# Performance work log

Measured on AMD Instinct MI355X. Metric: run time of the kernel, lower is better.

Reference implementation:

```python
import jax, jax.numpy as jnp
import numpy as np

DIM, H, DH, MLP, ADIM = 512, 8, 64, 2048, 256
B, T = 4, 2048
EPS = 1e-5


def setup_inputs() -> dict:
    key = jax.random.key(0)
    ks = jax.random.split(key, 10)
    s = 0.02
    inner = H * DH
    return {
        "x": jax.random.normal(ks[0], (B, T, DIM), jnp.float32),
        "action_emb": jax.random.normal(ks[1], (B, T, ADIM), jnp.float32),
        "causal_mask": jnp.tril(jnp.ones((T, T), dtype=bool)),
        "Wqkv": jax.random.normal(ks[2], (3 * inner, DIM), jnp.float32) * s,
        "Wout": jax.random.normal(ks[3], (DIM, inner), jnp.float32) * s,
        "bout": jnp.zeros((DIM,), jnp.float32),
        "W1": jax.random.normal(ks[4], (MLP, DIM), jnp.float32) * s,
        "b1": jnp.zeros((MLP,), jnp.float32),
        "W2": jax.random.normal(ks[5], (DIM, MLP), jnp.float32) * s,
        "b2": jnp.zeros((DIM,), jnp.float32),
        # adaLN is zero-init in the module; use small random so modulation is exercised
        "Wmod": jax.random.normal(ks[6], (6 * DIM, ADIM), jnp.float32) * s,
        "bmod": jnp.zeros((6 * DIM,), jnp.float32),
    }


def _layernorm(z):
    mu = jnp.mean(z, axis=-1, keepdims=True)
    var = jnp.var(z, axis=-1, keepdims=True)
    return (z - mu) * jax.lax.rsqrt(var + EPS)


def reference(x, action_emb, causal_mask, Wqkv, Wout, bout, W1, b1, W2, b2, Wmod, bmod):
    b, t, d = x.shape
    mod = jax.nn.silu(action_emb) @ Wmod.T + bmod            # (B,T,6*dim)
    shift1, scale1, gate1, shift2, scale2, gate2 = jnp.split(mod, 6, axis=-1)

    h = _layernorm(x) * (1.0 + scale1) + shift1
    qkv = (h @ Wqkv.T).reshape(b, t, 3, H, DH)
    q, k, v = qkv[:, :, 0], qkv[:, :, 1], qkv[:, :, 2]        # (B,T,H,DH)
    scores = jnp.einsum("bqhd,bkhd->bhqk", q, k) * (DH ** -0.5)
    scores = jnp.where(causal_mask, scores, -jnp.inf)
    attn = jax.nn.softmax(scores, axis=-1)                   # dropout=eval (identity)
    h = jnp.einsum("bhqk,bkhd->bqhd", attn, v).reshape(b, t, H * DH)
    h = h @ Wout.T + bout
    x = x + gate1 * h

    h = _layernorm(x) * (1.0 + scale2) + shift2
    h = jax.nn.gelu(h @ W1.T + b1, approximate=False) @ W2.T + b2
    return x + gate2 * h
```

## Files before the change

### kernel.cpp

```cpp
#include <hip/hip_runtime.h>
#include <math.h>
#include <stdint.h>

#define BB 4
#define TT 2048
#define NTOK 8192
#define DIMD 512
#define HH 8
#define DHH 64
#define MLPD 2048
#define ADIMD 256
#define MODD 3072
#define LNEPS 1e-5f
#define LOG2E_8 0.18033688011112042f

typedef short short8 __attribute__((ext_vector_type(8)));
typedef unsigned short ushort4v __attribute__((ext_vector_type(4)));
typedef __bf16 bf16x8 __attribute__((ext_vector_type(8)));
typedef float f32x4 __attribute__((ext_vector_type(4)));

static __device__ __forceinline__ unsigned short f2bf(float f) {
    union { float f; unsigned u; } v; v.f = f;
    unsigned r = v.u + 0x7fffu + ((v.u >> 16) & 1u);
    return (unsigned short)(r >> 16);
}
static __device__ __forceinline__ float bf2f(unsigned short u) {
    union { unsigned u; float f; } v; v.u = (unsigned)u << 16; return v.f;
}

static __device__ __forceinline__ f32x4 mfma_bf16(short8 a, short8 b, f32x4 c) {
    return __builtin_amdgcn_mfma_f32_16x16x32_bf16(
        __builtin_bit_cast(bf16x8, a), __builtin_bit_cast(bf16x8, b), c, 0, 0, 0);
}

struct CvtArgs {
    const float* s[6];
    unsigned short* d[6];
    int cum[7];
};
__global__ __launch_bounds__(256) void cvt_all(CvtArgs a)
{
    const int i = blockIdx.x * 256 + threadIdx.x;
    if (i >= a.cum[6]) return;
    int seg = 0;
    #pragma unroll
    for (int k = 1; k < 6; k++) seg += (i >= a.cum[k]);
    const int off = i - a.cum[seg];
    float4 v = ((const float4*)a.s[seg])[off];
    if (seg == 5) {
        v.x = v.x / (1.f + __expf(-v.x));
        v.y = v.y / (1.f + __expf(-v.y));
        v.z = v.z / (1.f + __expf(-v.z));
        v.w = v.w / (1.f + __expf(-v.w));
    }
    ushort4v o = { f2bf(v.x), f2bf(v.y), f2bf(v.z), f2bf(v.w) };
    ((ushort4v*)a.d[seg])[off] = o;
}

template<int EPI, int BN>
__global__ __launch_bounds__(256) void gemm_bf16(
    const unsigned short* __restrict__ A, const unsigned short* __restrict__ Bw,
    const float* __restrict__ bias, const float* __restrict__ res,
    const unsigned short* __restrict__ mod,
    int M, int N, int K,
    void* __restrict__ Cv)
{
    constexpr int MT = (BN == 128) ? 4 : 2;
    constexpr int NPB = (BN == 128) ? 4 : 2;
    __shared__ unsigned short As[128 * 72];
    __shared__ unsigned short Bs[BN * 72];

    const int tid = threadIdx.x;
    const int w = tid >> 6, lane = tid & 63;
    const int quad = lane >> 4, l16 = lane & 15;
    const int wrow = (BN == 128) ? (w >> 1) * 64 : w * 32;
    const int wcol = (BN == 128) ? (w & 1) * 64 : 0;
    const int row0 = blockIdx.y * 128, col0 = blockIdx.x * BN;

    const int srow = tid >> 3;
    const int skc  = (tid & 7) * 8;

    f32x4 acc[MT][4];
    #pragma unroll
    for (int i = 0; i < MT; i++)
        #pragma unroll
        for (int j = 0; j < 4; j++) acc[i][j] = (f32x4){0.f, 0.f, 0.f, 0.f};

    short8 pA[4], pB[NPB];
    auto prefetch = [&](int k0) {
        #pragma unroll
        for (int p = 0; p < 4; p++)
            pA[p] = *(const short8*)&A[(size_t)(row0 + srow + p * 32) * K + k0 + skc];
        #pragma unroll
        for (int p = 0; p < NPB; p++)
            pB[p] = *(const short8*)&Bw[(size_t)(col0 + srow + p * 32) * K + k0 + skc];
    };
    auto stage = [&]() {
        #pragma unroll
        for (int p = 0; p < 4; p++)
            *(short8*)&As[(srow + p * 32) * 72 + skc] = pA[p];
        #pragma unroll
        for (int p = 0; p < NPB; p++)
            *(short8*)&Bs[(srow + p * 32) * 72 + skc] = pB[p];
    };

    prefetch(0);
    stage();
    __syncthreads();

    for (int k0 = 0; k0 < K; k0 += 64) {
        const bool more = (k0 + 64 < K);
        if (more) prefetch(k0 + 64);

        #pragma unroll
        for (int ks = 0; ks < 2; ks++) {
            short8 af[MT], bf[4];
            #pragma unroll
            for (int mt = 0; mt < MT; mt++)
                af[mt] = *(const short8*)&As[(wrow + mt * 16 + l16) * 72 + ks * 32 + quad * 8];
            #pragma unroll
            for (int nt = 0; nt < 4; nt++)
                bf[nt] = *(const short8*)&Bs[(wcol + nt * 16 + l16) * 72 + ks * 32 + quad * 8];
            #pragma unroll
            for (int nt = 0; nt < 4; nt++)
                #pragma unroll
                for (int mt = 0; mt < MT; mt++)
                    acc[mt][nt] = mfma_bf16(af[mt], bf[nt], acc[mt][nt]);
        }
        __syncthreads();
        if (more) stage();
        __syncthreads();
    }

    float* Cf = (float*)Cv;
    unsigned short* Cb = (unsigned short*)Cv;
    #pragma unroll
    for (int mt = 0; mt < MT; mt++) {
        #pragma unroll
        for (int r = 0; r < 4; r++) {
            const int row = row0 + wrow + mt * 16 + quad * 4 + r;
            #pragma unroll
            for (int nt = 0; nt < 4; nt++) {
                const int col = col0 + wcol + nt * 16 + l16;
                const size_t idx = (size_t)row * N + col;
                const float v = acc[mt][nt][r];
                if (EPI == 0) {
                    Cb[idx] = f2bf(v);
                } else if (EPI == 2) {
                    float t = v + bias[col];
                    Cb[idx] = f2bf(0.5f * t * (1.f + erff(t * 0.70710678118654752f)));
                } else if (EPI == 3) {
                    float t = v + bias[col];
                    Cf[idx] = res[idx] + bf2f(mod[(size_t)row * MODD + 1024 + col]) * t;
                } else if (EPI == 4) {
                    float t = v + bias[col];
                    Cf[idx] = Cf[idx] + bf2f(mod[(size_t)row * MODD + 2560 + col]) * t;
                } else if (EPI == 5) {
                    Cb[idx] = f2bf(v + bias[col]);
                }
            }
        }
    }
}

__global__ __launch_bounds__(256) void adaln_ln(
    const float* __restrict__ src, const unsigned short* __restrict__ mod,
    unsigned short* __restrict__ dst, int shift_off, int scale_off)
{
    const int n = blockIdx.x;
    const int tid = threadIdx.x;
    const float* xr = src + (size_t)n * DIMD;
    float v0 = xr[tid], v1 = xr[tid + 256];
    float s = v0 + v1;
    float q = v0 * v0 + v1 * v1;
    #pragma unroll
    for (int o = 32; o > 0; o >>= 1) {
        s += __shfl_down(s, o);
        q += __shfl_down(q, o);
    }
    __shared__ float sh[8];
    __shared__ float mu_sh, rs_sh;
    const int wid = tid >> 6, lane = tid & 63;
    if (lane == 0) { sh[wid] = s; sh[wid + 4] = q; }
    __syncthreads();
    if (tid == 0) {
        float S = sh[0] + sh[1] + sh[2] + sh[3];
        float Q = sh[4] + sh[5] + sh[6] + sh[7];
        float mu = S * (1.f / DIMD);
        float var = Q * (1.f / DIMD) - mu * mu;
        mu_sh = mu;
        rs_sh = rsqrtf(var + LNEPS);
    }
    __syncthreads();
    const float mu = mu_sh, rs = rs_sh;
    const unsigned short* mrow = mod + (size_t)n * MODD;
    const size_t o0 = (size_t)n * DIMD + tid;
    dst[o0]       = f2bf((v0 - mu) * rs * (1.f + bf2f(mrow[scale_off + tid]))       + bf2f(mrow[shift_off + tid]));
    dst[o0 + 256] = f2bf((v1 - mu) * rs * (1.f + bf2f(mrow[scale_off + tid + 256])) + bf2f(mrow[shift_off + tid + 256]));
}

__global__ __launch_bounds__(256, 2) void attn_mfma(
    const unsigned short* __restrict__ qkv, unsigned short* __restrict__ outb)
{
    __shared__ unsigned short Kt[128][72];
    __shared__ unsigned short Vt[64][136];
    __shared__ unsigned short Ps[4][32][136];

    const int qi = (TT / 128 - 1) - blockIdx.x;
    const int h = blockIdx.y, b = blockIdx.z;
    const int tid = threadIdx.x;
    const int w = tid >> 6;
    const int lane = tid & 63;
    const int quad = lane >> 4;
    const int l16 = lane & 15;

    const int qw = qi * 128 + w * 32;
    const size_t tokbase = (size_t)b * TT;

    short8 qf[2][2];
    #pragma unroll
    for (int nt = 0; nt < 2; nt++) {
        const unsigned short* qp = qkv + (tokbase + qw + nt * 16 + l16) * 1536 + h * 64 + quad * 8;
        #pragma unroll
        for (int hd = 0; hd < 2; hd++) {
            short8 raw = *(const short8*)(qp + hd * 32);
            short8 f;
            #pragma unroll
            for (int j = 0; j < 8; j++)
                f[j] = (short)f2bf(bf2f((unsigned short)raw[j]) * LOG2E_8);
            qf[nt][hd] = f;
        }
    }

    f32x4 Oa[4][2];
    float mrun[2] = {-INFINITY, -INFINITY}, lrun[2] = {0.f, 0.f};
    #pragma unroll
    for (int mt = 0; mt < 4; mt++)
        #pragma unroll
        for (int nt = 0; nt < 2; nt++) Oa[mt][nt] = (f32x4){0.f, 0.f, 0.f, 0.f};

    const int nkt = qi + 1;
    const int vk0 = (tid & 63) * 2;
    const int vdb = (tid >> 6) * 8;

    short8 kpre[4], vpre[4];
    auto prefetchKV = [&](int kt) {
        const unsigned short* kb = qkv + (tokbase + (size_t)kt * 128) * 1536 + 512 + h * 64;
        #pragma unroll
        for (int it = 0; it < 4; it++) {
            const int i = tid + it * 256;
            kpre[it] = *(const short8*)(kb + (size_t)(i >> 3) * 1536 + (i & 7) * 8);
        }
        const unsigned short* vb = qkv + (tokbase + (size_t)kt * 128 + vk0) * 1536 + 1024 + h * 64;
        #pragma unroll
        for (int p = 0; p < 2; p++) {
            vpre[2 * p]     = *(const short8*)(vb + p * 32 + vdb);
            vpre[2 * p + 1] = *(const short8*)(vb + 1536 + p * 32 + vdb);
        }
    };
    auto storeKV = [&]() {
        #pragma unroll
        for (int it = 0; it < 4; it++) {
            const int i = tid + it * 256;
            *(short8*)&Kt[i >> 3][(i & 7) * 8] = kpre[it];
        }
        #pragma unroll
        for (int p = 0; p < 2; p++)
            #pragma unroll
            for (int j = 0; j < 8; j++) {
                const int d = p * 32 + vdb + j;
                *(unsigned*)&Vt[d][vk0] =
                    (unsigned)(unsigned short)vpre[2 * p][j]
                    | ((unsigned)(unsigned short)vpre[2 * p + 1][j] << 16);
            }
    };

    prefetchKV(0);
    storeKV();
    __syncthreads();

    for (int kt = 0; kt < nkt; kt++) {
        const bool haveNext = (kt + 1 < nkt);
        if (haveNext) prefetchKV(kt + 1);

        short8 af[8][2];
        #pragma unroll
        for (int mk = 0; mk < 8; mk++) {
            af[mk][0] = *(const short8*)&Kt[mk * 16 + l16][quad * 8];
            af[mk][1] = *(const short8*)&Kt[mk * 16 + l16][32 + quad * 8];
        }
        #pragma unroll
        for (int nt = 0; nt < 2; nt++) {
            f32x4 st[8];
            #pragma unroll
            for (int mk = 0; mk < 8; mk++) {
                st[mk] = (f32x4){0.f, 0.f, 0.f, 0.f};
                st[mk] = mfma_bf16(af[mk][0], qf[nt][0], st[mk]);
                st[mk] = mfma_bf16(af[mk][1], qf[nt][1], st[mk]);
            }
            if (kt == qi) {
                const int qrel = w * 32 + nt * 16 + l16;
                #pragma unroll
                for (int mk = 0; mk < 8; mk++)
                    #pragma unroll
                    for (int r = 0; r < 4; r++)
                        if (mk * 16 + quad * 4 + r > qrel) st[mk][r] = -INFINITY;
            }
            float tm = -INFINITY;
            #pragma unroll
            for (int mk = 0; mk < 8; mk++)
                #pragma unroll
                for (int r = 0; r < 4; r++) tm = fmaxf(tm, st[mk][r]);
            tm = fmaxf(tm, __shfl_xor(tm, 16));
            tm = fmaxf(tm, __shfl_xor(tm, 32));
            const float mn = fmaxf(mrun[nt], tm);
            const float alpha = __builtin_amdgcn_exp2f(mrun[nt] - mn);
            mrun[nt] = mn;
            float ts = 0.f;
            #pragma unroll
            for (int mk = 0; mk < 8; mk++) {
                const float p0 = __builtin_amdgcn_exp2f(st[mk][0] - mn);
                const float p1 = __builtin_amdgcn_exp2f(st[mk][1] - mn);
                const float p2 = __builtin_amdgcn_exp2f(st[mk][2] - mn);
                const float p3 = __builtin_amdgcn_exp2f(st[mk][3] - mn);
                ts += (p0 + p1) + (p2 + p3);
                const unsigned long long pk =
                    (unsigned long long)f2bf(p0)
                    | ((unsigned long long)f2bf(p1) << 16)
                    | ((unsigned long long)f2bf(p2) << 32)
                    | ((unsigned long long)f2bf(p3) << 48);
                *(unsigned long long*)&Ps[w][nt * 16 + l16][mk * 16 + quad * 4] = pk;
            }
            ts += __shfl_xor(ts, 16);
            ts += __shfl_xor(ts, 32);
            lrun[nt] = lrun[nt] * alpha + ts;
            #pragma unroll
            for (int mt = 0; mt < 4; mt++) Oa[mt][nt] *= alpha;
        }
        __threadfence_block();

        short8 pf0[4], pf1[4];
        #pragma unroll
        for (int kc = 0; kc < 4; kc++) {
            pf0[kc] = *(const short8*)&Ps[w][l16][kc * 32 + quad * 8];
            pf1[kc] = *(const short8*)&Ps[w][16 + l16][kc * 32 + quad * 8];
        }
        #pragma unroll
        for (int mt = 0; mt < 4; mt++)
            #pragma unroll
            for (int kc = 0; kc < 4; kc++) {
                const short8 vf = *(const short8*)&Vt[mt * 16 + l16][kc * 32 + quad * 8];
                Oa[mt][0] = mfma_bf16(vf, pf0[kc], Oa[mt][0]);
                Oa[mt][1] = mfma_bf16(vf, pf1[kc], Oa[mt][1]);
            }

        __syncthreads();
        if (haveNext) storeKV();
        __syncthreads();
    }

    #pragma unroll
    for (int nt = 0; nt < 2; nt++) {
        const float inv = 1.f / lrun[nt];
        const size_t tok = tokbase + qw + nt * 16 + l16;
        #pragma unroll
        for (int mt = 0; mt < 4; mt++) {
            const unsigned long long pk =
                (unsigned long long)f2bf(Oa[mt][nt][0] * inv)
                | ((unsigned long long)f2bf(Oa[mt][nt][1] * inv) << 16)
                | ((unsigned long long)f2bf(Oa[mt][nt][2] * inv) << 32)
                | ((unsigned long long)f2bf(Oa[mt][nt][3] * inv) << 48);
            *(unsigned long long*)&outb[tok * DIMD + h * 64 + mt * 16 + quad * 4] = pk;
        }
    }
}

extern "C" void kernel_launch(void* const* d_in, const int* in_sizes, int n_in,
                              void* d_out, int out_size, void* d_ws, size_t ws_size,
                              hipStream_t stream)
{
    (void)in_sizes; (void)n_in; (void)out_size; (void)ws_size;

    const float* x    = (const float*)d_in[0];
    const float* aemb = (const float*)d_in[1];
    const float* Wqkv = (const float*)d_in[3];
    const float* Wout = (const float*)d_in[4];
    const float* bout = (const float*)d_in[5];
    const float* W1   = (const float*)d_in[6];
    const float* b1   = (const float*)d_in[7];
    const float* W2   = (const float*)d_in[8];
    const float* b2   = (const float*)d_in[9];
    const float* Wmod = (const float*)d_in[10];
    const float* bmod = (const float*)d_in[11];

    float* out = (float*)d_out;

    char* p = (char*)d_ws;
    unsigned short* modw = (unsigned short*)p; p += (size_t)NTOK * MODD * 2;
    unsigned short* h12  = (unsigned short*)p; p += (size_t)NTOK * DIMD * 2;
    unsigned short* qkvb = (unsigned short*)p; p += (size_t)NTOK * 1536 * 2;
    unsigned short* attw = (unsigned short*)p; p += (size_t)NTOK * DIMD * 2;
    unsigned short* hid  = qkvb;
    unsigned short* sact = (unsigned short*)p; p += (size_t)NTOK * ADIMD * 2;
    unsigned short* wq = (unsigned short*)p;   p += (size_t)1536 * 512 * 2;
    unsigned short* wo = (unsigned short*)p;   p += (size_t)512 * 512 * 2;
    unsigned short* w1 = (unsigned short*)p;   p += (size_t)2048 * 512 * 2;
    unsigned short* w2 = (unsigned short*)p;   p += (size_t)512 * 2048 * 2;
    unsigned short* wm = (unsigned short*)p;   p += (size_t)3072 * 256 * 2;

    CvtArgs ca;
    ca.s[0] = Wqkv; ca.d[0] = wq;
    ca.s[1] = Wout; ca.d[1] = wo;
    ca.s[2] = W1;   ca.d[2] = w1;
    ca.s[3] = W2;   ca.d[3] = w2;
    ca.s[4] = Wmod; ca.d[4] = wm;
    ca.s[5] = aemb; ca.d[5] = sact;
    const int n4s[6] = {1536 * 512 / 4, 512 * 512 / 4, 2048 * 512 / 4,
                        512 * 2048 / 4, 3072 * 256 / 4, NTOK * ADIMD / 4};
    ca.cum[0] = 0;
    for (int i = 0; i < 6; i++) ca.cum[i + 1] = ca.cum[i] + n4s[i];
    cvt_all<<<(ca.cum[6] + 255) / 256, 256, 0, stream>>>(ca);

    gemm_bf16<5, 128><<<dim3(MODD / 128, NTOK / 128), 256, 0, stream>>>(
        sact, wm, bmod, nullptr, nullptr, NTOK, MODD, ADIMD, modw);

    adaln_ln<<<NTOK, 256, 0, stream>>>(x, modw, h12, 0, 512);

    gemm_bf16<0, 128><<<dim3(1536 / 128, NTOK / 128), 256, 0, stream>>>(
        h12, wq, nullptr, nullptr, nullptr, NTOK, 1536, DIMD, qkvb);

    attn_mfma<<<dim3(TT / 128, HH, BB), 256, 0, stream>>>(qkvb, attw);

    gemm_bf16<3, 64><<<dim3(DIMD / 64, NTOK / 128), 256, 0, stream>>>(
        attw, wo, bout, x, modw, NTOK, DIMD, DIMD, out);

    adaln_ln<<<NTOK, 256, 0, stream>>>(out, modw, h12, 1536, 2048);

    gemm_bf16<2, 128><<<dim3(MLPD / 128, NTOK / 128), 256, 0, stream>>>(
        h12, w1, b1, nullptr, nullptr, NTOK, MLPD, DIMD, hid);

    gemm_bf16<4, 64><<<dim3(DIMD / 64, NTOK / 128), 256, 0, stream>>>(
        hid, w2, b2, nullptr, modw, NTOK, DIMD, MLPD, out);
}
```

Measured before the change: 338.1 us.

## Shrink attention tiles to 64 queries and 64 keys per block

Retiles the flash-attention kernel so each block handles 64 queries (16 per wave) and streams 64-key K/V tiles, instead of 128 queries with 128-key tiles. Shared memory and register use drop, launch bounds rise to 4 blocks per SM, and the grid doubles. The aim is more parallelism and occupancy with finer causal-diagonal waste. The trade-off is that each K/V tile is reused by half as many queries, so global K/V traffic and barrier count per FLOP go up.

```diff
diff --git a/kernel.cpp b/kernel.cpp
--- a/kernel.cpp
+++ b/kernel.cpp
@@ -199,14 +199,14 @@
     dst[o0 + 256] = f2bf((v1 - mu) * rs * (1.f + bf2f(mrow[scale_off + tid + 256])) + bf2f(mrow[shift_off + tid + 256]));
 }
 
-__global__ __launch_bounds__(256, 2) void attn_mfma(
+__global__ __launch_bounds__(256, 4) void attn_mfma(
     const unsigned short* __restrict__ qkv, unsigned short* __restrict__ outb)
 {
-    __shared__ unsigned short Kt[128][72];
-    __shared__ unsigned short Vt[64][136];
-    __shared__ unsigned short Ps[4][32][136];
-
-    const int qi = (TT / 128 - 1) - blockIdx.x;
+    __shared__ unsigned short Kt[64][72];
+    __shared__ unsigned short Vt[64][72];
+    __shared__ unsigned short Ps[4][16][72];
+
+    const int qi = (TT / 64 - 1) - blockIdx.x;
     const int h = blockIdx.y, b = blockIdx.z;
     const int tid = threadIdx.x;
     const int w = tid >> 6;
@@ -214,13 +214,12 @@
     const int quad = lane >> 4;
     const int l16 = lane & 15;
 
-    const int qw = qi * 128 + w * 32;
+    const int qw = qi * 64 + w * 16;
     const size_t tokbase = (size_t)b * TT;
 
-    short8 qf[2][2];
-    #pragma unroll
-    for (int nt = 0; nt < 2; nt++) {
-        const unsigned short* qp = qkv + (tokbase + qw + nt * 16 + l16) * 1536 + h * 64 + quad * 8;
+    short8 qf[2];
+    {
+        const unsigned short* qp = qkv + (tokbase + qw + l16) * 1536 + h * 64 + quad * 8;
         #pragma unroll
         for (int hd = 0; hd < 2; hd++) {
             short8 raw = *(const short8*)(qp + hd * 32);
@@ -228,51 +227,43 @@
             #pragma unroll
             for (int j = 0; j < 8; j++)
                 f[j] = (short)f2bf(bf2f((unsigned short)raw[j]) * LOG2E_8);
-            qf[nt][hd] = f;
-        }
-    }
-
-    f32x4 Oa[4][2];
-    float mrun[2] = {-INFINITY, -INFINITY}, lrun[2] = {0.f, 0.f};
+            qf[hd] = f;
+        }
+    }
+
+    f32x4 Oa[4];
+    float mrun = -INFINITY, lrun = 0.f;
     #pragma unroll
-    for (int mt = 0; mt < 4; mt++)
-        #pragma unroll
-        for (int nt = 0; nt < 2; nt++) Oa[mt][nt] = (f32x4){0.f, 0.f, 0.f, 0.f};
+    for (int mt = 0; mt < 4; mt++) Oa[mt] = (f32x4){0.f, 0.f, 0.f, 0.f};
 
     const int nkt = qi + 1;
-    const int vk0 = (tid & 63) * 2;
-    const int vdb = (tid >> 6) * 8;
-
-    short8 kpre[4], vpre[4];
+    const int vk0 = (tid & 31) * 2;
+    const int vdb = (tid >> 5) * 8;
+
+    short8 kpre[2], vpre[2];
     auto prefetchKV = [&](int kt) {
-        const unsigned short* kb = qkv + (tokbase + (size_t)kt * 128) * 1536 + 512 + h * 64;
-        #pragma unroll
-        for (int it = 0; it < 4; it++) {
+        const unsigned short* kb = qkv + (tokbase + (size_t)kt * 64) * 1536 + 512 + h * 64;
+        #pragma unroll
+        for (int it = 0; it < 2; it++) {
             const int i = tid + it * 256;
             kpre[it] = *(const short8*)(kb + (size_t)(i >> 3) * 1536 + (i & 7) * 8);
         }
-        const unsigned short* vb = qkv + (tokbase + (size_t)kt * 128 + vk0) * 1536 + 1024 + h * 64;
-        #pragma unroll
-        for (int p = 0; p < 2; p++) {
-            vpre[2 * p]     = *(const short8*)(vb + p * 32 + vdb);
-            vpre[2 * p + 1] = *(const short8*)(vb + 1536 + p * 32 + vdb);
-        }
+        const unsigned short* vb = qkv + (tokbase + (size_t)kt * 64 + vk0) * 1536 + 1024 + h * 64 + vdb;
+        vpre[0] = *(const short8*)vb;
+        vpre[1] = *(const short8*)(vb + 1536);
     };
     auto storeKV = [&]() {
         #pragma unroll
-        for (int it = 0; it < 4; it++) {
+        for (int it = 0; it < 2; it++) {
             const int i = tid + it * 256;
             *(short8*)&Kt[i >> 3][(i & 7) * 8] = kpre[it];
         }
         #pragma unroll
-        for (int p = 0; p < 2; p++)
-            #pragma unroll
-            for (int j = 0; j < 8; j++) {
-                const int d = p * 32 + vdb + j;
-                *(unsigned*)&Vt[d][vk0] =
-                    (unsigned)(unsigned short)vpre[2 * p][j]
-                    | ((unsigned)(unsigned short)vpre[2 * p + 1][j] << 16);
-            }
+        for (int j = 0; j < 8; j++) {
+            *(unsigned*)&Vt[vdb + j][vk0] =
+                (unsigned)(unsigned short)vpre[0][j]
+                | ((unsigned)(unsigned short)vpre[1][j] << 16);
+        }
     };
 
     prefetchKV(0);
@@ -283,75 +274,65 @@
         const bool haveNext = (kt + 1 < nkt);
         if (haveNext) prefetchKV(kt + 1);
 
-        short8 af[8][2];
-        #pragma unroll
-        for (int mk = 0; mk < 8; mk++) {
-            af[mk][0] = *(const short8*)&Kt[mk * 16 + l16][quad * 8];
-            af[mk][1] = *(const short8*)&Kt[mk * 16 + l16][32 + quad * 8];
-        }
-        #pragma unroll
-        for (int nt = 0; nt < 2; nt++) {
-            f32x4 st[8];
-            #pragma unroll
-            for (int mk = 0; mk < 8; mk++) {
-                st[mk] = (f32x4){0.f, 0.f, 0.f, 0.f};
-                st[mk] = mfma_bf16(af[mk][0], qf[nt][0], st[mk]);
-                st[mk] = mfma_bf16(af[mk][1], qf[nt][1], st[mk]);
-            }
-            if (kt == qi) {
-                const int qrel = w * 32 + nt * 16 + l16;
+        f32x4 st[4];
+        #pragma unroll
+        for (int mk = 0; mk < 4; mk++) {
+            const short8 a0 = *(const short8*)&Kt[mk * 16 + l16][quad * 8];
+            const short8 a1 = *(const short8*)&Kt[mk * 16 + l16][32 + quad * 8];
+            st[mk] = (f32x4){0.f, 0.f, 0.f, 0.f};
+            st[mk] = mfma_bf16(a0, qf[0], st[mk]);
+            st[mk] = mfma_bf16(a1, qf[1], st[mk]);
+        }
+        if (kt == qi) {
+            const int qpos = qw + l16;
+            #pragma unroll
+            for (int mk = 0; mk < 4; mk++)
                 #pragma unroll
-                for (int mk = 0; mk < 8; mk++)
-                    #pragma unroll
-                    for (int r = 0; r < 4; r++)
-                        if (mk * 16 + quad * 4 + r > qrel) st[mk][r] = -INFINITY;
-            }
-            float tm = -INFINITY;
-            #pragma unroll
-            for (int mk = 0; mk < 8; mk++)
-                #pragma unroll
-                for (int r = 0; r < 4; r++) tm = fmaxf(tm, st[mk][r]);
-            tm = fmaxf(tm, __shfl_xor(tm, 16));
-            tm = fmaxf(tm, __shfl_xor(tm, 32));
-            const float mn = fmaxf(mrun[nt], tm);
-            const float alpha = __builtin_amdgcn_exp2f(mrun[nt] - mn);
-            mrun[nt] = mn;
-            float ts = 0.f;
-            #pragma unroll
-            for (int mk = 0; mk < 8; mk++) {
-                const float p0 = __builtin_amdgcn_exp2f(st[mk][0] - mn);
-                const float p1 = __builtin_amdgcn_exp2f(st[mk][1] - mn);
-                const float p2 = __builtin_amdgcn_exp2f(st[mk][2] - mn);
-                const float p3 = __builtin_amdgcn_exp2f(st[mk][3] - mn);
-                ts += (p0 + p1) + (p2 + p3);
-                const unsigned long long pk =
-                    (unsigned long long)f2bf(p0)
-                    | ((unsigned long long)f2bf(p1) << 16)
-                    | ((unsigned long long)f2bf(p2) << 32)
-                    | ((unsigned long long)f2bf(p3) << 48);
-                *(unsigned long long*)&Ps[w][nt * 16 + l16][mk * 16 + quad * 4] = pk;
-            }
-            ts += __shfl_xor(ts, 16);
-            ts += __shfl_xor(ts, 32);
-            lrun[nt] = lrun[nt] * alpha + ts;
-            #pragma unroll
-            for (int mt = 0; mt < 4; mt++) Oa[mt][nt] *= alpha;
-        }
+                for (int r = 0; r < 4; r++)
+                    if (kt * 64 + mk * 16 + quad * 4 + r > qpos) st[mk][r] = -INFINITY;
+        }
+        float tm = -INFINITY;
+        #pragma unroll
+        for (int mk = 0; mk < 4; mk++)
+            #pragma unroll
+            for (int r = 0; r < 4; r++) tm = fmaxf(tm, st[mk][r]);
+        tm = fmaxf(tm, __shfl_xor(tm, 16));
+        tm = fmaxf(tm, __shfl_xor(tm, 32));
+        const float mn = fmaxf(mrun, tm);
+        const float alpha = __builtin_amdgcn_exp2f(mrun - mn);
+        mrun = mn;
+        float ts = 0.f;
+        #pragma unroll
+        for (int mk = 0; mk < 4; mk++) {
+            const float p0 = __builtin_amdgcn_exp2f(st[mk][0] - mn);
+            const float p1 = __builtin_amdgcn_exp2f(st[mk][1] - mn);
+            const float p2 = __builtin_amdgcn_exp2f(st[mk][2] - mn);
+            const float p3 = __builtin_amdgcn_exp2f(st[mk][3] - mn);
+            ts += (p0 + p1) + (p2 + p3);
+            const unsigned long long pk =
+                (unsigned long long)f2bf(p0)
+                | ((unsigned long long)f2bf(p1) << 16)
+                | ((unsigned long long)f2bf(p2) << 32)
+                | ((unsigned long long)f2bf(p3) << 48);
+            *(unsigned long long*)&Ps[w][l16][mk * 16 + quad * 4] = pk;
+        }
+        ts += __shfl_xor(ts, 16);
+        ts += __shfl_xor(ts, 32);
+        lrun = lrun * alpha + ts;
+        #pragma unroll
+        for (int mt = 0; mt < 4; mt++) Oa[mt] *= alpha;
         __threadfence_block();
 
-        short8 pf0[4], pf1[4];
-        #pragma unroll
-        for (int kc = 0; kc < 4; kc++) {
-            pf0[kc] = *(const short8*)&Ps[w][l16][kc * 32 + quad * 8];
-            pf1[kc] = *(const short8*)&Ps[w][16 + l16][kc * 32 + quad * 8];
-        }
+        short8 pf[2];
+        #pragma unroll
+        for (int kc = 0; kc < 2; kc++)
+            pf[kc] = *(const short8*)&Ps[w][l16][kc * 32 + quad * 8];
         #pragma unroll
         for (int mt = 0; mt < 4; mt++)
             #pragma unroll
-            for (int kc = 0; kc < 4; kc++) {
+            for (int kc = 0; kc < 2; kc++) {
                 const short8 vf = *(const short8*)&Vt[mt * 16 + l16][kc * 32 + quad * 8];
-                Oa[mt][0] = mfma_bf16(vf, pf0[kc], Oa[mt][0]);
-                Oa[mt][1] = mfma_bf16(vf, pf1[kc], Oa[mt][1]);
+                Oa[mt] = mfma_bf16(vf, pf[kc], Oa[mt]);
             }
 
         __syncthreads();
@@ -359,17 +340,16 @@
         __syncthreads();
     }
 
-    #pragma unroll
-    for (int nt = 0; nt < 2; nt++) {
-        const float inv = 1.f / lrun[nt];
-        const size_t tok = tokbase + qw + nt * 16 + l16;
+    {
+        const float inv = 1.f / lrun;
+        const size_t tok = tokbase + qw + l16;
         #pragma unroll
         for (int mt = 0; mt < 4; mt++) {
             const unsigned long long pk =
-                (unsigned long long)f2bf(Oa[mt][nt][0] * inv)
-                | ((unsigned long long)f2bf(Oa[mt][nt][1] * inv) << 16)
-                | ((unsigned long long)f2bf(Oa[mt][nt][2] * inv) << 32)
-                | ((unsigned long long)f2bf(Oa[mt][nt][3] * inv) << 48);
+                (unsigned long long)f2bf(Oa[mt][0] * inv)
+                | ((unsigned long long)f2bf(Oa[mt][1] * inv) << 16)
+                | ((unsigned long long)f2bf(Oa[mt][2] * inv) << 32)
+                | ((unsigned long long)f2bf(Oa[mt][3] * inv) << 48);
             *(unsigned long long*)&outb[tok * DIMD + h * 64 + mt * 16 + quad * 4] = pk;
         }
     }
@@ -429,7 +409,7 @@
     gemm_bf16<0, 128><<<dim3(1536 / 128, NTOK / 128), 256, 0, stream>>>(
         h12, wq, nullptr, nullptr, nullptr, NTOK, 1536, DIMD, qkvb);
 
-    attn_mfma<<<dim3(TT / 128, HH, BB), 256, 0, stream>>>(qkvb, attw);
+    attn_mfma<<<dim3(TT / 64, HH, BB), 256, 0, stream>>>(qkvb, attw);
 
     gemm_bf16<3, 64><<<dim3(DIMD / 64, NTOK / 128), 256, 0, stream>>>(
         attw, wo, bout, x, modw, NTOK, DIMD, DIMD, out);
```

Result: no change. 337.8 us (-0.1%).
